# Kernel optimization log

Hardware: AMD Instinct MI355X
Metric: run time of the kernel (lower is better)

## Reference

```python
import jax, jax.numpy as jnp
import numpy as np

NUM_HEADS = 12
EMB = 768
D_KEY = 64
D_VALUE = 64
MASKED = True


def setup_inputs() -> dict:
    key = jax.random.key(0)
    k1, k2, k3, k4 = jax.random.split(key, 4)
    x = jax.random.normal(k1, (1, 4096, EMB), dtype=jnp.float32)
    q_proj = jax.random.normal(k2, (NUM_HEADS, EMB, D_KEY), dtype=jnp.float32)
    k_proj = jax.random.normal(k3, (NUM_HEADS, EMB, D_KEY), dtype=jnp.float32)
    v_proj = jax.random.normal(k4, (NUM_HEADS, EMB, D_VALUE), dtype=jnp.float32)
    return {"x": x, "q_proj": q_proj, "k_proj": k_proj, "v_proj": v_proj}


def reference(x, q_proj, k_proj, v_proj):
    # x: [B, S, E]; projections: [H, E, dk/dv]
    q = jnp.einsum("bse,hek->bhsk", x, q_proj)  # [B,H,S,dk]
    k = jnp.einsum("bse,hek->bhsk", x, k_proj)  # [B,H,S,dk]
    v = jnp.einsum("bse,hev->bhsv", x, v_proj)  # [B,H,S,dv]
    scale = jnp.sqrt(jnp.asarray(D_KEY, dtype=x.dtype))
    scores = jnp.einsum("bhsk,bhtk->bhst", q, k) / scale  # [B,H,S,S]
    if MASKED:
        S = x.shape[1]
        # causal mask: disallow attending to future positions (strict upper triangle)
        mask = jnp.triu(jnp.ones((S, S), dtype=bool), k=1)
        scores = jnp.where(mask, -jnp.inf, scores)
    attn = jax.nn.softmax(scores, axis=-1)
    out = jnp.einsum("bhst,bhtv->bhsv", attn, v)  # [B,H,S,dv]
    return out
```

## Files before the change

kernel.cpp:

```cpp
#include <hip/hip_runtime.h>
#include <hip/hip_bf16.h>

#define NH 12
#define SEQ 4096
#define E 768
#define DK 64

typedef float f32x4 __attribute__((ext_vector_type(4)));
typedef float f32x16 __attribute__((ext_vector_type(16)));
typedef __bf16 bf16x8 __attribute__((ext_vector_type(8)));
typedef __bf16 bf16x4 __attribute__((ext_vector_type(4)));
typedef unsigned u32x2 __attribute__((ext_vector_type(2)));
typedef unsigned u32x4 __attribute__((ext_vector_type(4)));

#define MFMA16(a, b, c) __builtin_amdgcn_mfma_f32_16x16x32_bf16((a), (b), (c), 0, 0, 0)
#define MFMA32(a, b, c) __builtin_amdgcn_mfma_f32_32x32x16_bf16((a), (b), (c), 0, 0, 0)

#define SCL 0.18033688011112042f
#define DEFER 10.8f

#define PART_SZ 4352

__device__ __forceinline__ void gload16(const void* g, void* l) {
    __builtin_amdgcn_global_load_lds(
        (const __attribute__((address_space(1))) void*)g,
        (__attribute__((address_space(3))) void*)l, 16, 0, 0);
}

__device__ __forceinline__ void block_sync() {
    __builtin_amdgcn_sched_barrier(0);
    __builtin_amdgcn_s_barrier();
    __builtin_amdgcn_sched_barrier(0);
}

__device__ __forceinline__ unsigned cvtpk(float lo, float hi) {
    unsigned r;
    asm("v_cvt_pk_bf16_f32 %0, %1, %2" : "=v"(r) : "v"(lo), "v"(hi));
    return r;
}
__device__ __forceinline__ u32x2 plswap(unsigned a, unsigned b) {
    return __builtin_amdgcn_permlane32_swap(a, b, false, false);
}
__device__ __forceinline__ float xhalf_max(float v) {
    u32x2 r = plswap(__float_as_uint(v), __float_as_uint(v));
    return fmaxf(__uint_as_float(r.x), __uint_as_float(r.y));
}
__device__ __forceinline__ float xhalf_add(float v) {
    u32x2 r = plswap(__float_as_uint(v), __float_as_uint(v));
    return __uint_as_float(r.x) + __uint_as_float(r.y);
}

__global__ __launch_bounds__(256) void xsplit_kernel(const float* __restrict__ x,
                                                     __bf16* __restrict__ xh,
                                                     __bf16* __restrict__ xl) {
    int i = blockIdx.x * blockDim.x + threadIdx.x;
    float4 v = ((const float4*)x)[i];
    bf16x4 h, l;
    float vv[4] = {v.x, v.y, v.z, v.w};
#pragma unroll
    for (int j = 0; j < 4; ++j) {
        __bf16 hh = (__bf16)vv[j];
        h[j] = hh;
        l[j] = (__bf16)(vv[j] - (float)hh);
    }
    ((bf16x4*)xh)[i] = h;
    ((bf16x4*)xl)[i] = l;
}

__global__ void wsplit_kernel(const float* __restrict__ qp,
                              const float* __restrict__ kp,
                              const float* __restrict__ vp,
                              __bf16* __restrict__ wtq_h, __bf16* __restrict__ wtq_l,
                              __bf16* __restrict__ wtk_h, __bf16* __restrict__ wtk_l,
                              __bf16* __restrict__ wtv_h) {
    int idx = blockIdx.x * blockDim.x + threadIdx.x;
    if (idx >= NH * E * DK) return;
    int h = idx / (E * DK);
    int rem = idx - h * E * DK;
    int k = rem / DK;
    int n = rem - k * DK;
    int o = h * DK * E + n * E + k;
    float q = qp[idx];
    __bf16 qh = (__bf16)q;
    wtq_h[o] = qh;
    wtq_l[o] = (__bf16)(q - (float)qh);
    float kk = kp[idx] * SCL;
    __bf16 kh = (__bf16)kk;
    wtk_h[o] = kh;
    wtk_l[o] = (__bf16)(kk - (float)kh);
    wtv_h[o] = (__bf16)vp[idx];
}

__global__ __launch_bounds__(256, 2) void proj_kernel(
    const __bf16* __restrict__ xh, const __bf16* __restrict__ xl,
    const __bf16* __restrict__ wq_h_g, const __bf16* __restrict__ wq_l_g,
    const __bf16* __restrict__ wk_h_g, const __bf16* __restrict__ wk_l_g,
    const __bf16* __restrict__ wv_g,
    __bf16* __restrict__ qh_o, __bf16* __restrict__ ql_o,
    __bf16* __restrict__ kh_o, __bf16* __restrict__ kl_o,
    __bf16* __restrict__ vt_o) {
    __shared__ char wlds[2][20480];

    const int wg = (blockIdx.x & 7) * 96 + (blockIdx.x >> 3);
    const int head = wg >> 6;
    const int rb = wg & 63;
    const int wave = threadIdx.x >> 6;
    const int lane = threadIdx.x & 63;
    const int lrow = lane & 15;
    const int lk8 = (lane >> 4) * 8;
    const int g4 = (lane >> 4) * 4;
    const int rowbase = rb * 64 + wave * 16;

    const char* bases[5] = {
        (const char*)(wq_h_g + head * DK * E), (const char*)(wq_l_g + head * DK * E),
        (const char*)(wk_h_g + head * DK * E), (const char*)(wk_l_g + head * DK * E),
        (const char*)(wv_g + head * DK * E)};
    const int srow = lane >> 2;
    const int scol = (lane & 3) * 16;

    auto STAGE = [&](int buf, int ks) {
#pragma unroll
        for (int r = 0; r < 5; ++r) {
            int q = wave * 5 + r;
            const char* src = bases[q >> 2] + (size_t)((q & 3) * 16 + srow) * (E * 2) + ks * 64 + scol;
            gload16(src, wlds[buf] + q * 1024 + lane * 16);
        }
    };

    f32x4 accq[4], acck[4], accv[4];
#pragma unroll
    for (int f = 0; f < 4; ++f) {
        accq[f] = (f32x4){0.f, 0.f, 0.f, 0.f};
        acck[f] = (f32x4){0.f, 0.f, 0.f, 0.f};
        accv[f] = (f32x4){0.f, 0.f, 0.f, 0.f};
    }

    bf16x8 ah, al, ahn, aln;
    auto LOADA = [&](int ks, bf16x8& h, bf16x8& l) {
        size_t xo = (size_t)(rowbase + lrow) * E + ks * 32 + lk8;
        h = *(const bf16x8*)(xh + xo);
        l = *(const bf16x8*)(xl + xo);
    };

    LOADA(0, ah, al);
    STAGE(0, 0);
    int buf = 0;
    for (int ks = 0; ks < 24; ++ks) {
        if (ks < 23) {
            LOADA(ks + 1, ahn, aln);
            STAGE(buf ^ 1, ks + 1);
            asm volatile("s_waitcnt vmcnt(7)" ::: "memory");
        } else {
            asm volatile("s_waitcnt vmcnt(0)" ::: "memory");
        }
        block_sync();
#pragma unroll
        for (int f = 0; f < 4; ++f) {
            int bo = (f * 16 + lrow) * 64 + lk8 * 2;
            bf16x8 bqh = *(const bf16x8*)(wlds[buf] + bo);
            bf16x8 bql = *(const bf16x8*)(wlds[buf] + 4096 + bo);
            bf16x8 bkh = *(const bf16x8*)(wlds[buf] + 8192 + bo);
            bf16x8 bkl = *(const bf16x8*)(wlds[buf] + 12288 + bo);
            bf16x8 bv  = *(const bf16x8*)(wlds[buf] + 16384 + bo);
            accq[f] = MFMA16(ah, bqh, accq[f]);
            accq[f] = MFMA16(ah, bql, accq[f]);
            accq[f] = MFMA16(al, bqh, accq[f]);
            acck[f] = MFMA16(ah, bkh, acck[f]);
            acck[f] = MFMA16(ah, bkl, acck[f]);
            acck[f] = MFMA16(al, bkh, acck[f]);
            accv[f] = MFMA16(bv, ah, accv[f]);
        }
        block_sync();
        if (ks < 23) {
            ah = ahn;
            al = aln;
        }
        buf ^= 1;
    }

    char* khb = (char*)kh_o + (size_t)head * SEQ * DK * 2;
    char* klb = (char*)kl_o + (size_t)head * SEQ * DK * 2;
    char* vb = (char*)vt_o + (size_t)head * DK * SEQ * 2;
#pragma unroll
    for (int f = 0; f < 4; ++f)
#pragma unroll
        for (int r = 0; r < 4; ++r) {
            int srow_o = rowbase + g4 + r;
            int d = f * 16 + lrow;
            size_t o = (size_t)head * SEQ * DK + (size_t)srow_o * DK + d;
            float qv = accq[f][r];
            __bf16 qhh = (__bf16)qv;
            qh_o[o] = qhh;
            ql_o[o] = (__bf16)(qv - (float)qhh);
            size_t ko = (size_t)(srow_o >> 6) * 8192 + ((srow_o >> 5) & 1) * 4096
                      + (size_t)f * 1024
                      + ((srow_o & 31) + 32 * ((lrow >> 3) & 1)) * 16 + (lrow & 7) * 2;
            float kv = acck[f][r];
            __bf16 khh = (__bf16)kv;
            *(__bf16*)(khb + ko) = khh;
            *(__bf16*)(klb + ko) = (__bf16)(kv - (float)khh);
            int vd = f * 16 + g4 + r;
            int vs = rowbase + lrow;
            size_t vo = (size_t)(vs >> 6) * 8192 + ((vd >> 5) & 1) * 4096
                      + ((vs >> 4) & 3) * 1024
                      + ((vd & 31) + 32 * ((vs >> 3) & 1)) * 16 + (vs & 7) * 2;
            *(__bf16*)(vb + vo) = (__bf16)accv[f][r];
        }
}

__global__ __launch_bounds__(256, 2) void attn_part_kernel(
    const __bf16* __restrict__ qh, const __bf16* __restrict__ ql,
    const __bf16* __restrict__ kh, const __bf16* __restrict__ kl,
    const __bf16* __restrict__ vt,
    char* __restrict__ part, int fine, int perx) {
    const int blk = (blockIdx.x & 7) * perx + (blockIdx.x >> 3);
    const int wave = threadIdx.x >> 6;
    const int task = blk * 4 + wave;
    const int lane = threadIdx.x & 63;
    const int lq = lane & 31;
    const int lh = lane >> 5;

    const int G = fine ? 16 : 32;
    const int gmax = fine ? 7 : 3;
    const int tph = fine ? 576 : 320;

    const int head = task / tph;
    const int t = task - head * tph;
    int g = 0;
#pragma unroll 8
    for (int gg = 1; gg <= 7; ++gg)
        if (gg <= gmax && t >= G * gg * (gg + 1) / 2) g = gg;
    const int nsp = g + 1;
    const int u = t - G * g * (g + 1) / 2;
    const int w = G * g + u / nsp;
    const int split = u - (u / nsp) * nsp;
    const int ktot = (w >> 1) + 1;
    const int lo = (split * ktot) / nsp;
    const int hi = ((split + 1) * ktot) / nsp;
    const int rowbase = w * 32;

    const size_t hoff = (size_t)head * SEQ * DK;

    bf16x8 qBh[4], qBl[4];
    {
        const __bf16* qph = qh + hoff + (size_t)(rowbase + lq) * DK + lh * 8;
        const __bf16* qpl = ql + hoff + (size_t)(rowbase + lq) * DK + lh * 8;
#pragma unroll
        for (int ds = 0; ds < 4; ++ds) {
            qBh[ds] = *(const bf16x8*)(qph + ds * 16);
            qBl[ds] = *(const bf16x8*)(qpl + ds * 16);
        }
    }

    const char* kh_p = (const char*)(kh + hoff) + (size_t)lo * 8192 + lane * 16;
    const char* kl_p = (const char*)(kl + hoff) + (size_t)lo * 8192 + lane * 16;
    const char* vt_p = (const char*)(vt + (size_t)head * DK * SEQ) + (size_t)lo * 8192 + lane * 16;

    f32x16 O0 = (f32x16)0.0f, O1 = (f32x16)0.0f;
    float m = -3.0e38f, lsum = 0.f;

    for (int tt = lo; tt < hi; ++tt) {
        const int kb = tt * 64;

        f32x16 s0 = (f32x16)0.0f, s1 = (f32x16)0.0f;
#pragma unroll
        for (int ds = 0; ds < 4; ++ds) {
            bf16x8 ah0 = *(const bf16x8*)(kh_p + ds * 1024);
            bf16x8 al0 = *(const bf16x8*)(kl_p + ds * 1024);
            bf16x8 ah1 = *(const bf16x8*)(kh_p + 4096 + ds * 1024);
            bf16x8 al1 = *(const bf16x8*)(kl_p + 4096 + ds * 1024);
            s0 = MFMA32(ah0, qBh[ds], s0);
            s1 = MFMA32(ah1, qBh[ds], s1);
            s0 = MFMA32(al0, qBh[ds], s0);
            s1 = MFMA32(al1, qBh[ds], s1);
            s0 = MFMA32(ah0, qBl[ds], s0);
            s1 = MFMA32(ah1, qBl[ds], s1);
        }

        bf16x8 v00 = *(const bf16x8*)(vt_p + 0);
        bf16x8 v01 = *(const bf16x8*)(vt_p + 1024);
        bf16x8 v10 = *(const bf16x8*)(vt_p + 2048);
        bf16x8 v11 = *(const bf16x8*)(vt_p + 3072);
        bf16x8 w00 = *(const bf16x8*)(vt_p + 4096);
        bf16x8 w01 = *(const bf16x8*)(vt_p + 5120);
        bf16x8 w10 = *(const bf16x8*)(vt_p + 6144);
        bf16x8 w11 = *(const bf16x8*)(vt_p + 7168);

        if (kb + 63 > rowbase) {
            int qa = rowbase + lq;
#pragma unroll
            for (int r = 0; r < 16; ++r) {
                int kp = kb + ((r & 3) + 8 * (r >> 2) + 4 * lh);
                if (kp > qa) s0[r] = -1.0e30f;
                if (kp + 32 > qa) s1[r] = -1.0e30f;
            }
        }

        float x0 = fmaxf(s0[0], s0[1]), x1 = fmaxf(s0[2], s0[3]);
        float x2 = fmaxf(s0[4], s0[5]), x3 = fmaxf(s0[6], s0[7]);
#pragma unroll
        for (int r = 8; r < 16; r += 4) {
            x0 = fmaxf(x0, fmaxf(s0[r], s0[r + 1]));
            x1 = fmaxf(x1, fmaxf(s0[r + 2], s0[r + 3]));
        }
#pragma unroll
        for (int r = 0; r < 16; r += 4) {
            x2 = fmaxf(x2, fmaxf(s1[r], s1[r + 1]));
            x3 = fmaxf(x3, fmaxf(s1[r + 2], s1[r + 3]));
        }
        float mx = xhalf_max(fmaxf(fmaxf(x0, x1), fmaxf(x2, x3)));

        if (!__all(mx - m <= DEFER)) {
            float mn = fmaxf(m, mx);
            float al = exp2f(m - mn);
            m = mn;
            lsum *= al;
#pragma unroll
            for (int r = 0; r < 16; ++r) {
                float a = __shfl(al, (r & 3) + 8 * (r >> 2) + 4 * lh);
                O0[r] *= a;
                O1[r] *= a;
            }
        }

        s0 = s0 - m;
        s1 = s1 - m;
#pragma unroll
        for (int r = 0; r < 16; ++r) {
            s0[r] = exp2f(s0[r]);
            s1[r] = exp2f(s1[r]);
        }
        {
            f32x16 sv = s0 + s1;
            float p0 = 0.f, p1 = 0.f;
#pragma unroll
            for (int r = 0; r < 16; r += 4) {
                p0 += sv[r] + sv[r + 1];
                p1 += sv[r + 2] + sv[r + 3];
            }
            lsum += p0 + p1;
        }

        unsigned W0 = cvtpk(s0[0], s0[1]), W1 = cvtpk(s0[2], s0[3]);
        unsigned W2 = cvtpk(s0[4], s0[5]), W3 = cvtpk(s0[6], s0[7]);
        unsigned W4 = cvtpk(s0[8], s0[9]), W5 = cvtpk(s0[10], s0[11]);
        unsigned W6 = cvtpk(s0[12], s0[13]), W7 = cvtpk(s0[14], s0[15]);
        u32x2 rA = plswap(W0, W2), rB = plswap(W1, W3);
        u32x2 rC = plswap(W4, W6), rD = plswap(W5, W7);
        bf16x8 p00 = __builtin_bit_cast(bf16x8, (u32x4){rA.x, rB.x, rA.y, rB.y});
        bf16x8 p01 = __builtin_bit_cast(bf16x8, (u32x4){rC.x, rD.x, rC.y, rD.y});
        W0 = cvtpk(s1[0], s1[1]); W1 = cvtpk(s1[2], s1[3]);
        W2 = cvtpk(s1[4], s1[5]); W3 = cvtpk(s1[6], s1[7]);
        W4 = cvtpk(s1[8], s1[9]); W5 = cvtpk(s1[10], s1[11]);
        W6 = cvtpk(s1[12], s1[13]); W7 = cvtpk(s1[14], s1[15]);
        rA = plswap(W0, W2); rB = plswap(W1, W3);
        rC = plswap(W4, W6); rD = plswap(W5, W7);
        bf16x8 p10 = __builtin_bit_cast(bf16x8, (u32x4){rA.x, rB.x, rA.y, rB.y});
        bf16x8 p11 = __builtin_bit_cast(bf16x8, (u32x4){rC.x, rD.x, rC.y, rD.y});

        O0 = MFMA32(p00, v00, O0);
        O0 = MFMA32(p01, v01, O0);
        O0 = MFMA32(p10, v10, O0);
        O0 = MFMA32(p11, v11, O0);
        O1 = MFMA32(p00, w00, O1);
        O1 = MFMA32(p01, w01, O1);
        O1 = MFMA32(p10, w10, O1);
        O1 = MFMA32(p11, w11, O1);

        kh_p += 8192;
        kl_p += 8192;
        vt_p += 8192;
    }

    char* pb = part + (size_t)task * PART_SZ;
    unsigned* ph = (unsigned*)pb;
#pragma unroll
    for (int r = 0; r < 16; r += 2) {
        ph[(r >> 1) * 64 + lane] = cvtpk(O0[r], O0[r + 1]);
        ph[512 + (r >> 1) * 64 + lane] = cvtpk(O1[r], O1[r + 1]);
    }
    float lf = xhalf_add(lsum);
    float* pm = (float*)(pb + 4096);
    if (lane < 32) {
        pm[lq] = m;
        pm[32 + lq] = lf;
    }
}

__global__ __launch_bounds__(256) void attn_comb_kernel(
    const char* __restrict__ part, float* __restrict__ out, int fine) {
    const int W = blockIdx.x;
    const int head = W >> 7, w = W & 127;
    const int G = fine ? 16 : 32;
    const int tph = fine ? 576 : 320;
    const int g = w / G;
    const int nsp = g + 1;
    const int tb = head * tph + G * g * (g + 1) / 2 + (w - G * g) * nsp;

    const int tid = threadIdx.x;
    const int row = tid >> 3;
    const int d0 = (tid & 7) * 8;
    const int lane0 = (d0 & 31) + 32 * ((row >> 2) & 1);
    const int r = (row & 3) + 4 * (row >> 3);
    const int word = (r >> 1) * 64;
    const int hi16 = r & 1;
    const char* p0 = part + (size_t)tb * PART_SZ;

    float mstar = -3.0e38f;
    for (int s = 0; s < nsp; ++s) {
        const float* pm = (const float*)(p0 + s * PART_SZ + 4096);
        mstar = fmaxf(mstar, pm[row]);
    }

    float acc[8] = {0.f, 0.f, 0.f, 0.f, 0.f, 0.f, 0.f, 0.f};
    float lt = 0.f;
    for (int s = 0; s < nsp; ++s) {
        const float* pm = (const float*)(p0 + s * PART_SZ + 4096);
        float wgt = exp2f(pm[row] - mstar);
        lt += wgt * pm[32 + row];
        const unsigned* pw = (const unsigned*)(p0 + s * PART_SZ + (d0 >> 5) * 2048);
        u32x4 a = *(const u32x4*)(pw + word + lane0);
        u32x4 b = *(const u32x4*)(pw + word + lane0 + 4);
#pragma unroll
        for (int j = 0; j < 8; ++j) {
            unsigned u = (j < 4) ? a[j] : b[j - 4];
            unsigned bits = hi16 ? (u & 0xffff0000u) : (u << 16);
            acc[j] += wgt * __uint_as_float(bits);
        }
    }
    float inv = 1.0f / lt;
    size_t o = (size_t)head * SEQ * DK + (size_t)(w * 32 + row) * DK + d0;
#pragma unroll
    for (int j = 0; j < 8; ++j) out[o + j] = acc[j] * inv;
}

extern "C" void kernel_launch(void* const* d_in, const int* in_sizes, int n_in,
                              void* d_out, int out_size, void* d_ws, size_t ws_size,
                              hipStream_t stream) {
    const float* x = (const float*)d_in[0];
    const float* qp = (const float*)d_in[1];
    const float* kp = (const float*)d_in[2];
    const float* vp = (const float*)d_in[3];
    float* out = (float*)d_out;

    const size_t WT_SZ = (size_t)NH * DK * E * 2;
    const size_t QKV_SZ = (size_t)NH * SEQ * DK * 2;
    const size_t X_SZ = (size_t)SEQ * E * 2;
    char* ws = (char*)d_ws;
    __bf16* wtq_h = (__bf16*)(ws + 0 * WT_SZ);
    __bf16* wtq_l = (__bf16*)(ws + 1 * WT_SZ);
    __bf16* wtk_h = (__bf16*)(ws + 2 * WT_SZ);
    __bf16* wtk_l = (__bf16*)(ws + 3 * WT_SZ);
    __bf16* wtv_h = (__bf16*)(ws + 4 * WT_SZ);
    char* px = ws + 5 * WT_SZ;
    __bf16* xh = (__bf16*)(px + 0 * X_SZ);
    __bf16* xl = (__bf16*)(px + 1 * X_SZ);
    char* p2 = px + 2 * X_SZ;
    __bf16* qh = (__bf16*)(p2 + 0 * QKV_SZ);
    __bf16* ql = (__bf16*)(p2 + 1 * QKV_SZ);
    __bf16* kh = (__bf16*)(p2 + 2 * QKV_SZ);
    __bf16* kl = (__bf16*)(p2 + 3 * QKV_SZ);
    __bf16* vt = (__bf16*)(p2 + 4 * QKV_SZ);
    char* tail = p2 + 5 * QKV_SZ;

    const size_t need = (size_t)(p2 - ws) + 5 * QKV_SZ + 6912ull * PART_SZ;
    const int fine = (ws_size >= need) ? 1 : 0;
    char* part = fine ? tail : ws;
    const int nblk = fine ? 1728 : 960;
    const int perx = fine ? 216 : 120;

    hipLaunchKernelGGL(xsplit_kernel, dim3(SEQ * E / 4 / 256), dim3(256), 0, stream,
                       x, xh, xl);
    hipLaunchKernelGGL(wsplit_kernel, dim3((NH * E * DK + 255) / 256), dim3(256), 0, stream,
                       qp, kp, vp, wtq_h, wtq_l, wtk_h, wtk_l, wtv_h);
    hipLaunchKernelGGL(proj_kernel, dim3(768), dim3(256), 0, stream,
                       xh, xl, wtq_h, wtq_l, wtk_h, wtk_l, wtv_h, qh, ql, kh, kl, vt);
    hipLaunchKernelGGL(attn_part_kernel, dim3(nblk), dim3(256), 0, stream,
                       qh, ql, kh, kl, vt, part, fine, perx);
    hipLaunchKernelGGL(attn_comb_kernel, dim3(1536), dim3(256), 0, stream,
                       part, out, fine);
}
```

Measured before the change: 169.3 us.

## Share K/V tiles across waves via double-buffered LDS staging with new split schedule

The attention kernel now gives each block four adjacent 32-row query tiles of one head. The block cooperatively stages each 64-key K-high, K-low and V tile into double-buffered LDS with async global-to-LDS loads, instead of each wave reading K/V straight from global memory. Work is re-split so block groups get a split count that grows with depth, and block order is reversed so the longest tasks start first. The combine kernel indexing is updated to match. This adds block barriers per tile and idle iterations for waves whose rows sit above the diagonal. It also drops the fallback for a small workspace.

```diff
diff --git a/kernel.cpp b/kernel.cpp
--- a/kernel.cpp
+++ b/kernel.cpp
@@ -20,6 +20,7 @@
 #define DEFER 10.8f
 
 #define PART_SZ 4352
+#define TPH 144
 
 __device__ __forceinline__ void gload16(const void* g, void* l) {
     __builtin_amdgcn_global_load_lds(
@@ -212,32 +213,29 @@
     const __bf16* __restrict__ qh, const __bf16* __restrict__ ql,
     const __bf16* __restrict__ kh, const __bf16* __restrict__ kl,
     const __bf16* __restrict__ vt,
-    char* __restrict__ part, int fine, int perx) {
-    const int blk = (blockIdx.x & 7) * perx + (blockIdx.x >> 3);
+    char* __restrict__ part) {
+    __shared__ char kvlds[2][24576];
+
+    const int blk = (blockIdx.x & 7) * 216 + (blockIdx.x >> 3);
+    const int head = blk / TPH;
+    const int t = TPH - 1 - (blk - head * TPH);
+    int g = 0, base = 0;
+    for (int gg = 1; gg < 32; ++gg) {
+        int qq = gg >> 2, rr = gg & 3;
+        int b = 2 * qq * (qq + 1) + rr * (qq + 1);
+        if (t >= b) { g = gg; base = b; }
+    }
+    const int s = t - base;
+    const int nsp = (g + 4) >> 2;
+    const int ktot = 2 * g + 2;
+    const int lo = (s * ktot) / nsp;
+    const int hi = ((s + 1) * ktot) / nsp;
+
     const int wave = threadIdx.x >> 6;
-    const int task = blk * 4 + wave;
     const int lane = threadIdx.x & 63;
     const int lq = lane & 31;
     const int lh = lane >> 5;
-
-    const int G = fine ? 16 : 32;
-    const int gmax = fine ? 7 : 3;
-    const int tph = fine ? 576 : 320;
-
-    const int head = task / tph;
-    const int t = task - head * tph;
-    int g = 0;
-#pragma unroll 8
-    for (int gg = 1; gg <= 7; ++gg)
-        if (gg <= gmax && t >= G * gg * (gg + 1) / 2) g = gg;
-    const int nsp = g + 1;
-    const int u = t - G * g * (g + 1) / 2;
-    const int w = G * g + u / nsp;
-    const int split = u - (u / nsp) * nsp;
-    const int ktot = (w >> 1) + 1;
-    const int lo = (split * ktot) / nsp;
-    const int hi = ((split + 1) * ktot) / nsp;
-    const int rowbase = w * 32;
+    const int rowbase = (4 * g + wave) * 32;
 
     const size_t hoff = (size_t)head * SEQ * DK;
 
@@ -251,128 +249,156 @@
             qBl[ds] = *(const bf16x8*)(qpl + ds * 16);
         }
     }
-
-    const char* kh_p = (const char*)(kh + hoff) + (size_t)lo * 8192 + lane * 16;
-    const char* kl_p = (const char*)(kl + hoff) + (size_t)lo * 8192 + lane * 16;
-    const char* vt_p = (const char*)(vt + (size_t)head * DK * SEQ) + (size_t)lo * 8192 + lane * 16;
+    asm volatile("s_waitcnt vmcnt(0)" ::: "memory");
+
+    const char* kh_b = (const char*)(kh + hoff);
+    const char* kl_b = (const char*)(kl + hoff);
+    const char* vt_b = (const char*)(vt + (size_t)head * DK * SEQ);
+
+    auto STAGE = [&](int buf, int tile) {
+#pragma unroll
+        for (int r = 0; r < 6; ++r) {
+            int q = wave * 6 + r;
+            const char* src;
+            if (q < 8)       src = kh_b + (size_t)tile * 8192 + q * 1024;
+            else if (q < 16) src = kl_b + (size_t)tile * 8192 + (q - 8) * 1024;
+            else             src = vt_b + (size_t)tile * 8192 + (q - 16) * 1024;
+            gload16(src + lane * 16, kvlds[buf] + q * 1024);
+        }
+    };
 
     f32x16 O0 = (f32x16)0.0f, O1 = (f32x16)0.0f;
     float m = -3.0e38f, lsum = 0.f;
 
+    STAGE(0, lo);
+    int buf = 0;
     for (int tt = lo; tt < hi; ++tt) {
+        if (tt + 1 < hi) {
+            STAGE(buf ^ 1, tt + 1);
+            asm volatile("s_waitcnt vmcnt(6)" ::: "memory");
+        } else {
+            asm volatile("s_waitcnt vmcnt(0)" ::: "memory");
+        }
+        block_sync();
+
         const int kb = tt * 64;
-
-        f32x16 s0 = (f32x16)0.0f, s1 = (f32x16)0.0f;
-#pragma unroll
-        for (int ds = 0; ds < 4; ++ds) {
-            bf16x8 ah0 = *(const bf16x8*)(kh_p + ds * 1024);
-            bf16x8 al0 = *(const bf16x8*)(kl_p + ds * 1024);
-            bf16x8 ah1 = *(const bf16x8*)(kh_p + 4096 + ds * 1024);
-            bf16x8 al1 = *(const bf16x8*)(kl_p + 4096 + ds * 1024);
-            s0 = MFMA32(ah0, qBh[ds], s0);
-            s1 = MFMA32(ah1, qBh[ds], s1);
-            s0 = MFMA32(al0, qBh[ds], s0);
-            s1 = MFMA32(al1, qBh[ds], s1);
-            s0 = MFMA32(ah0, qBl[ds], s0);
-            s1 = MFMA32(ah1, qBl[ds], s1);
-        }
-
-        bf16x8 v00 = *(const bf16x8*)(vt_p + 0);
-        bf16x8 v01 = *(const bf16x8*)(vt_p + 1024);
-        bf16x8 v10 = *(const bf16x8*)(vt_p + 2048);
-        bf16x8 v11 = *(const bf16x8*)(vt_p + 3072);
-        bf16x8 w00 = *(const bf16x8*)(vt_p + 4096);
-        bf16x8 w01 = *(const bf16x8*)(vt_p + 5120);
-        bf16x8 w10 = *(const bf16x8*)(vt_p + 6144);
-        bf16x8 w11 = *(const bf16x8*)(vt_p + 7168);
-
-        if (kb + 63 > rowbase) {
-            int qa = rowbase + lq;
+        if (kb <= rowbase + 31) {
+            const char* Khl = kvlds[buf];
+            const char* Kll = kvlds[buf] + 8192;
+            const char* Vtl = kvlds[buf] + 16384;
+
+            f32x16 s0 = (f32x16)0.0f, s1 = (f32x16)0.0f;
+#pragma unroll
+            for (int ds = 0; ds < 4; ++ds) {
+                bf16x8 ah0 = *(const bf16x8*)(Khl + ds * 1024 + lane * 16);
+                bf16x8 al0 = *(const bf16x8*)(Kll + ds * 1024 + lane * 16);
+                bf16x8 ah1 = *(const bf16x8*)(Khl + 4096 + ds * 1024 + lane * 16);
+                bf16x8 al1 = *(const bf16x8*)(Kll + 4096 + ds * 1024 + lane * 16);
+                s0 = MFMA32(ah0, qBh[ds], s0);
+                s1 = MFMA32(ah1, qBh[ds], s1);
+                s0 = MFMA32(al0, qBh[ds], s0);
+                s1 = MFMA32(al1, qBh[ds], s1);
+                s0 = MFMA32(ah0, qBl[ds], s0);
+                s1 = MFMA32(ah1, qBl[ds], s1);
+            }
+
+            if (kb + 63 > rowbase) {
+                int qa = rowbase + lq;
+#pragma unroll
+                for (int r = 0; r < 16; ++r) {
+                    int kp = kb + ((r & 3) + 8 * (r >> 2) + 4 * lh);
+                    if (kp > qa) s0[r] = -1.0e30f;
+                    if (kp + 32 > qa) s1[r] = -1.0e30f;
+                }
+            }
+
+            float x0 = fmaxf(s0[0], s0[1]), x1 = fmaxf(s0[2], s0[3]);
+            float x2 = fmaxf(s0[4], s0[5]), x3 = fmaxf(s0[6], s0[7]);
+#pragma unroll
+            for (int r = 8; r < 16; r += 4) {
+                x0 = fmaxf(x0, fmaxf(s0[r], s0[r + 1]));
+                x1 = fmaxf(x1, fmaxf(s0[r + 2], s0[r + 3]));
+            }
+#pragma unroll
+            for (int r = 0; r < 16; r += 4) {
+                x2 = fmaxf(x2, fmaxf(s1[r], s1[r + 1]));
+                x3 = fmaxf(x3, fmaxf(s1[r + 2], s1[r + 3]));
+            }
+            float mx = xhalf_max(fmaxf(fmaxf(x0, x1), fmaxf(x2, x3)));
+
+            if (!__all(mx - m <= DEFER)) {
+                float mn = fmaxf(m, mx);
+                float al = exp2f(m - mn);
+                m = mn;
+                lsum *= al;
+#pragma unroll
+                for (int r = 0; r < 16; ++r) {
+                    float a = __shfl(al, (r & 3) + 8 * (r >> 2) + 4 * lh);
+                    O0[r] *= a;
+                    O1[r] *= a;
+                }
+            }
+
+            s0 = s0 - m;
+            s1 = s1 - m;
 #pragma unroll
             for (int r = 0; r < 16; ++r) {
-                int kp = kb + ((r & 3) + 8 * (r >> 2) + 4 * lh);
-                if (kp > qa) s0[r] = -1.0e30f;
-                if (kp + 32 > qa) s1[r] = -1.0e30f;
-            }
-        }
-
-        float x0 = fmaxf(s0[0], s0[1]), x1 = fmaxf(s0[2], s0[3]);
-        float x2 = fmaxf(s0[4], s0[5]), x3 = fmaxf(s0[6], s0[7]);
-#pragma unroll
-        for (int r = 8; r < 16; r += 4) {
-            x0 = fmaxf(x0, fmaxf(s0[r], s0[r + 1]));
-            x1 = fmaxf(x1, fmaxf(s0[r + 2], s0[r + 3]));
-        }
-#pragma unroll
-        for (int r = 0; r < 16; r += 4) {
-            x2 = fmaxf(x2, fmaxf(s1[r], s1[r + 1]));
-            x3 = fmaxf(x3, fmaxf(s1[r + 2], s1[r + 3]));
-        }
-        float mx = xhalf_max(fmaxf(fmaxf(x0, x1), fmaxf(x2, x3)));
-
-        if (!__all(mx - m <= DEFER)) {
-            float mn = fmaxf(m, mx);
-            float al = exp2f(m - mn);
-            m = mn;
-            lsum *= al;
-#pragma unroll
-            for (int r = 0; r < 16; ++r) {
-                float a = __shfl(al, (r & 3) + 8 * (r >> 2) + 4 * lh);
-                O0[r] *= a;
-                O1[r] *= a;
-            }
-        }
-
-        s0 = s0 - m;
-        s1 = s1 - m;
-#pragma unroll
-        for (int r = 0; r < 16; ++r) {
-            s0[r] = exp2f(s0[r]);
-            s1[r] = exp2f(s1[r]);
-        }
-        {
-            f32x16 sv = s0 + s1;
-            float p0 = 0.f, p1 = 0.f;
-#pragma unroll
-            for (int r = 0; r < 16; r += 4) {
-                p0 += sv[r] + sv[r + 1];
-                p1 += sv[r + 2] + sv[r + 3];
-            }
-            lsum += p0 + p1;
-        }
-
-        unsigned W0 = cvtpk(s0[0], s0[1]), W1 = cvtpk(s0[2], s0[3]);
-        unsigned W2 = cvtpk(s0[4], s0[5]), W3 = cvtpk(s0[6], s0[7]);
-        unsigned W4 = cvtpk(s0[8], s0[9]), W5 = cvtpk(s0[10], s0[11]);
-        unsigned W6 = cvtpk(s0[12], s0[13]), W7 = cvtpk(s0[14], s0[15]);
-        u32x2 rA = plswap(W0, W2), rB = plswap(W1, W3);
-        u32x2 rC = plswap(W4, W6), rD = plswap(W5, W7);
-        bf16x8 p00 = __builtin_bit_cast(bf16x8, (u32x4){rA.x, rB.x, rA.y, rB.y});
-        bf16x8 p01 = __builtin_bit_cast(bf16x8, (u32x4){rC.x, rD.x, rC.y, rD.y});
-        W0 = cvtpk(s1[0], s1[1]); W1 = cvtpk(s1[2], s1[3]);
-        W2 = cvtpk(s1[4], s1[5]); W3 = cvtpk(s1[6], s1[7]);
-        W4 = cvtpk(s1[8], s1[9]); W5 = cvtpk(s1[10], s1[11]);
-        W6 = cvtpk(s1[12], s1[13]); W7 = cvtpk(s1[14], s1[15]);
-        rA = plswap(W0, W2); rB = plswap(W1, W3);
-        rC = plswap(W4, W6); rD = plswap(W5, W7);
-        bf16x8 p10 = __builtin_bit_cast(bf16x8, (u32x4){rA.x, rB.x, rA.y, rB.y});
-        bf16x8 p11 = __builtin_bit_cast(bf16x8, (u32x4){rC.x, rD.x, rC.y, rD.y});
-
-        O0 = MFMA32(p00, v00, O0);
-        O0 = MFMA32(p01, v01, O0);
-        O0 = MFMA32(p10, v10, O0);
-        O0 = MFMA32(p11, v11, O0);
-        O1 = MFMA32(p00, w00, O1);
-        O1 = MFMA32(p01, w01, O1);
-        O1 = MFMA32(p10, w10, O1);
-        O1 = MFMA32(p11, w11, O1);
-
-        kh_p += 8192;
-        kl_p += 8192;
-        vt_p += 8192;
-    }
-
-    char* pb = part + (size_t)task * PART_SZ;
+                s0[r] = exp2f(s0[r]);
+                s1[r] = exp2f(s1[r]);
+            }
+            {
+                f32x16 sv = s0 + s1;
+                float p0 = 0.f, p1 = 0.f;
+#pragma unroll
+                for (int r = 0; r < 16; r += 4) {
+                    p0 += sv[r] + sv[r + 1];
+                    p1 += sv[r + 2] + sv[r + 3];
+                }
+                lsum += p0 + p1;
+            }
+
+            unsigned W0 = cvtpk(s0[0], s0[1]), W1 = cvtpk(s0[2], s0[3]);
+            unsigned W2 = cvtpk(s0[4], s0[5]), W3 = cvtpk(s0[6], s0[7]);
+            unsigned W4 = cvtpk(s0[8], s0[9]), W5 = cvtpk(s0[10], s0[11]);
+            unsigned W6 = cvtpk(s0[12], s0[13]), W7 = cvtpk(s0[14], s0[15]);
+            u32x2 rA = plswap(W0, W2), rB = plswap(W1, W3);
+            u32x2 rC = plswap(W4, W6), rD = plswap(W5, W7);
+            bf16x8 p00 = __builtin_bit_cast(bf16x8, (u32x4){rA.x, rB.x, rA.y, rB.y});
+            bf16x8 p01 = __builtin_bit_cast(bf16x8, (u32x4){rC.x, rD.x, rC.y, rD.y});
+            W0 = cvtpk(s1[0], s1[1]); W1 = cvtpk(s1[2], s1[3]);
+            W2 = cvtpk(s1[4], s1[5]); W3 = cvtpk(s1[6], s1[7]);
+            W4 = cvtpk(s1[8], s1[9]); W5 = cvtpk(s1[10], s1[11]);
+            W6 = cvtpk(s1[12], s1[13]); W7 = cvtpk(s1[14], s1[15]);
+            rA = plswap(W0, W2); rB = plswap(W1, W3);
+            rC = plswap(W4, W6); rD = plswap(W5, W7);
+            bf16x8 p10 = __builtin_bit_cast(bf16x8, (u32x4){rA.x, rB.x, rA.y, rB.y});
+            bf16x8 p11 = __builtin_bit_cast(bf16x8, (u32x4){rC.x, rD.x, rC.y, rD.y});
+
+            {
+                bf16x8 v00 = *(const bf16x8*)(Vtl + 0 + lane * 16);
+                bf16x8 v01 = *(const bf16x8*)(Vtl + 1024 + lane * 16);
+                bf16x8 v10 = *(const bf16x8*)(Vtl + 2048 + lane * 16);
+                bf16x8 v11 = *(const bf16x8*)(Vtl + 3072 + lane * 16);
+                O0 = MFMA32(p00, v00, O0);
+                O0 = MFMA32(p01, v01, O0);
+                O0 = MFMA32(p10, v10, O0);
+                O0 = MFMA32(p11, v11, O0);
+                bf16x8 w00 = *(const bf16x8*)(Vtl + 4096 + lane * 16);
+                bf16x8 w01 = *(const bf16x8*)(Vtl + 5120 + lane * 16);
+                bf16x8 w10 = *(const bf16x8*)(Vtl + 6144 + lane * 16);
+                bf16x8 w11 = *(const bf16x8*)(Vtl + 7168 + lane * 16);
+                O1 = MFMA32(p00, w00, O1);
+                O1 = MFMA32(p01, w01, O1);
+                O1 = MFMA32(p10, w10, O1);
+                O1 = MFMA32(p11, w11, O1);
+            }
+        }
+
+        block_sync();
+        buf ^= 1;
+    }
+
+    char* pb = part + ((size_t)(head * TPH + t) * 4 + wave) * PART_SZ;
     unsigned* ph = (unsigned*)pb;
 #pragma unroll
     for (int r = 0; r < 16; r += 2) {
@@ -388,14 +414,13 @@
 }
 
 __global__ __launch_bounds__(256) void attn_comb_kernel(
-    const char* __restrict__ part, float* __restrict__ out, int fine) {
+    const char* __restrict__ part, float* __restrict__ out) {
     const int W = blockIdx.x;
     const int head = W >> 7, w = W & 127;
-    const int G = fine ? 16 : 32;
-    const int tph = fine ? 576 : 320;
-    const int g = w / G;
-    const int nsp = g + 1;
-    const int tb = head * tph + G * g * (g + 1) / 2 + (w - G * g) * nsp;
+    const int g = w >> 2;
+    const int qq = g >> 2, rr = g & 3;
+    const int base_g = 2 * qq * (qq + 1) + rr * (qq + 1);
+    const int nsp = (g + 4) >> 2;
 
     const int tid = threadIdx.x;
     const int row = tid >> 3;
@@ -404,21 +429,22 @@
     const int r = (row & 3) + 4 * (row >> 3);
     const int word = (r >> 1) * 64;
     const int hi16 = r & 1;
-    const char* p0 = part + (size_t)tb * PART_SZ;
+    const char* p0 = part + ((size_t)(head * TPH + base_g) * 4 + (w & 3)) * PART_SZ;
 
     float mstar = -3.0e38f;
     for (int s = 0; s < nsp; ++s) {
-        const float* pm = (const float*)(p0 + s * PART_SZ + 4096);
+        const float* pm = (const float*)(p0 + (size_t)s * 4 * PART_SZ + 4096);
         mstar = fmaxf(mstar, pm[row]);
     }
 
     float acc[8] = {0.f, 0.f, 0.f, 0.f, 0.f, 0.f, 0.f, 0.f};
     float lt = 0.f;
     for (int s = 0; s < nsp; ++s) {
-        const float* pm = (const float*)(p0 + s * PART_SZ + 4096);
+        const char* ps = p0 + (size_t)s * 4 * PART_SZ;
+        const float* pm = (const float*)(ps + 4096);
         float wgt = exp2f(pm[row] - mstar);
         lt += wgt * pm[32 + row];
-        const unsigned* pw = (const unsigned*)(p0 + s * PART_SZ + (d0 >> 5) * 2048);
+        const unsigned* pw = (const unsigned*)(ps + (d0 >> 5) * 2048);
         u32x4 a = *(const u32x4*)(pw + word + lane0);
         u32x4 b = *(const u32x4*)(pw + word + lane0 + 4);
 #pragma unroll
@@ -461,13 +487,7 @@
     __bf16* kh = (__bf16*)(p2 + 2 * QKV_SZ);
     __bf16* kl = (__bf16*)(p2 + 3 * QKV_SZ);
     __bf16* vt = (__bf16*)(p2 + 4 * QKV_SZ);
-    char* tail = p2 + 5 * QKV_SZ;
-
-    const size_t need = (size_t)(p2 - ws) + 5 * QKV_SZ + 6912ull * PART_SZ;
-    const int fine = (ws_size >= need) ? 1 : 0;
-    char* part = fine ? tail : ws;
-    const int nblk = fine ? 1728 : 960;
-    const int perx = fine ? 216 : 120;
+    char* part = p2 + 5 * QKV_SZ;
 
     hipLaunchKernelGGL(xsplit_kernel, dim3(SEQ * E / 4 / 256), dim3(256), 0, stream,
                        x, xh, xl);
@@ -475,8 +495,8 @@
                        qp, kp, vp, wtq_h, wtq_l, wtk_h, wtk_l, wtv_h);
     hipLaunchKernelGGL(proj_kernel, dim3(768), dim3(256), 0, stream,
                        xh, xl, wtq_h, wtq_l, wtk_h, wtk_l, wtv_h, qh, ql, kh, kl, vt);
-    hipLaunchKernelGGL(attn_part_kernel, dim3(nblk), dim3(256), 0, stream,
-                       qh, ql, kh, kl, vt, part, fine, perx);
+    hipLaunchKernelGGL(attn_part_kernel, dim3(1728), dim3(256), 0, stream,
+                       qh, ql, kh, kl, vt, part);
     hipLaunchKernelGGL(attn_comb_kernel, dim3(1536), dim3(256), 0, stream,
-                       part, out, fine);
-}
+                       part, out);
+}
```

After: 165.9 us. 1.02x faster.
